# Optimization experiments

Hardware: AMD Instinct MI355X
Metric: run time of the kernel (lower is better)

The kernel has to match this reference:

```python
import jax, jax.numpy as jnp
import numpy as np

NUM_TRACKS = [5313, 1643, 128, 0]
MAX_TRACKS = max(NUM_TRACKS)
EMBED_DIM = 1536
LN_EPS = 1e-5


def setup_inputs() -> dict:
    key = jax.random.key(0)
    ks = jax.random.split(key, 8)
    B, S, D = 4, 896, EMBED_DIM
    inp = {
        "x": jax.random.normal(ks[0], (B, S, D), dtype=jnp.float32),
        "head_idx": jax.random.randint(ks[1], (B,), 0, 4, dtype=jnp.int64) if jax.config.jax_enable_x64 else jax.random.randint(ks[1], (B,), 0, 4).astype(jnp.int32),
    }
    for i, n in enumerate([5313, 1643, 128]):
        inp[f"gamma{i}"] = jnp.ones((D,), jnp.float32)
        inp[f"beta{i}"] = jnp.zeros((D,), jnp.float32)
        inp[f"W{i}"] = jax.random.normal(ks[2 + i], (n, D), dtype=jnp.float32) * 0.02
        inp[f"b{i}"] = jnp.zeros((n,), jnp.float32)
    return inp


def _linear_head(x, gamma, beta, W, b):
    # LayerNormFP32 -> Linear -> softplus, cast back to orig dtype
    orig_dtype = x.dtype
    xf = x.astype(jnp.float32)
    mu = jnp.mean(xf, axis=-1, keepdims=True)
    var = jnp.var(xf, axis=-1, keepdims=True)  # biased, as torch LayerNorm
    xn = (xf - mu) * jax.lax.rsqrt(var + LN_EPS) * gamma + beta
    h = jax.nn.softplus(jnp.einsum("bsd,td->bst", xn, W) + b)
    return h.astype(orig_dtype)


def reference(x, head_idx, gamma0, beta0, W0, b0,
              gamma1, beta1, W1, b1, gamma2, beta2, W2, b2):
    params = [(gamma0, beta0, W0, b0),
              (gamma1, beta1, W1, b1),
              (gamma2, beta2, W2, b2),
              None]  # ZeroHead
    B, S, _ = x.shape
    logits = jnp.zeros((B, S, MAX_TRACKS), dtype=x.dtype)
    for i, p in enumerate(params):
        if p is None:
            padded = jnp.zeros((B, S, MAX_TRACKS), dtype=x.dtype)
        else:
            h = _linear_head(x, *p)  # [B, S, n_i]
            pad = MAX_TRACKS - h.shape[-1]
            padded = jnp.pad(h, ((0, 0), (0, 0), (0, pad))) if pad > 0 else h
        mask = (head_idx == i)[:, None, None]
        logits = jnp.where(mask, padded, logits)
    return logits
```

## Files before the change

### kernel.cpp

```cpp
#include <hip/hip_runtime.h>
#include <hip/hip_bf16.h>

#define EMBED 1536
#define SEQ   896
#define NOUT  5313

#define N0 5313
#define N1 1643
#define N2 128
#define W0OFF 0
#define W1OFF 5376
#define W2OFF 7040
#define PTOT  7168

#define LN_BLOCKS 1792
#define WC_BLOCKS 5376
#define GEMM_GRID 1280
#define BK 128

typedef __attribute__((ext_vector_type(8))) short bf16x8;
typedef __attribute__((ext_vector_type(4))) float f32x4;

__device__ __forceinline__ void gload_lds16(const void* g, void* l) {
    __builtin_amdgcn_global_load_lds(
        (const __attribute__((address_space(1))) void*)g,
        (__attribute__((address_space(3))) void*)l, 16, 0, 0);
}

__device__ __forceinline__ int tiles_of(int h) {
    return (h == 0) ? 42 : (h == 1) ? 13 : (h == 2) ? 1 : 0;
}
__device__ __forceinline__ int nrows_of(int h) {
    return (h == 0) ? N0 : (h == 1) ? N1 : (h == 2) ? N2 : 0;
}

__global__ __launch_bounds__(256) void prep_kernel(
    const float* __restrict__ x, const int* __restrict__ head_idx,
    const float* __restrict__ g0, const float* __restrict__ be0,
    const float* __restrict__ g1, const float* __restrict__ be1,
    const float* __restrict__ g2, const float* __restrict__ be2,
    const float* __restrict__ W0, const float* __restrict__ W1,
    const float* __restrict__ W2,
    __hip_bfloat16* __restrict__ xn, __hip_bfloat16* __restrict__ wpad)
{
    const int tid = threadIdx.x;

    if (blockIdx.x < LN_BLOCKS) {
        const int half = tid >> 7;
        const int lt   = tid & 127;
        const int row  = blockIdx.x * 2 + half;
        const int b    = row / SEQ;
        const int h    = head_idx[b];
        if (h == 3) return;

        const float* gamma = (h == 1) ? g1 : (h == 2) ? g2 : g0;
        const float* beta  = (h == 1) ? be1 : (h == 2) ? be2 : be0;
        const float* xr = x + (size_t)row * EMBED;

        float4 v[3];
        float sum = 0.f, sq = 0.f;
#pragma unroll
        for (int i = 0; i < 3; ++i) {
            v[i] = ((const float4*)xr)[lt + i * 128];
            sum += v[i].x + v[i].y + v[i].z + v[i].w;
            sq  += v[i].x * v[i].x + v[i].y * v[i].y + v[i].z * v[i].z + v[i].w * v[i].w;
        }
#pragma unroll
        for (int off = 32; off > 0; off >>= 1) {
            sum += __shfl_down(sum, off);
            sq  += __shfl_down(sq, off);
        }
        __shared__ float s_sum[4], s_sq[4];
        const int wave = tid >> 6, lane = tid & 63;
        if (lane == 0) { s_sum[wave] = sum; s_sq[wave] = sq; }
        __syncthreads();
        const int wb = half << 1;
        const float mu  = (s_sum[wb] + s_sum[wb + 1]) * (1.f / EMBED);
        const float var = (s_sq[wb] + s_sq[wb + 1]) * (1.f / EMBED) - mu * mu;
        const float rs  = rsqrtf(var + 1e-5f);

        __hip_bfloat16* xo = xn + (size_t)row * EMBED;
#pragma unroll
        for (int i = 0; i < 3; ++i) {
            const int idx = lt + i * 128;
            float4 gv = ((const float4*)gamma)[idx];
            float4 bv = ((const float4*)beta)[idx];
            union { __hip_bfloat16 h4[4]; short4 s4; } u;
            u.h4[0] = __float2bfloat16((v[i].x - mu) * rs * gv.x + bv.x);
            u.h4[1] = __float2bfloat16((v[i].y - mu) * rs * gv.y + bv.y);
            u.h4[2] = __float2bfloat16((v[i].z - mu) * rs * gv.z + bv.z);
            u.h4[3] = __float2bfloat16((v[i].w - mu) * rs * gv.w + bv.w);
            ((short4*)xo)[idx] = u.s4;
        }
    } else {
        const int gid = (blockIdx.x - LN_BLOCKS) * 256 + tid;
        const int r = gid / 192;
        const int c = (gid - r * 192) * 8;
        const int region = (r < W1OFF) ? 0 : (r < W2OFF) ? 1 : 2;
        const int h0 = head_idx[0], h1 = head_idx[1];
        const int h2 = head_idx[2], h3 = head_idx[3];
        if (region != h0 && region != h1 && region != h2 && region != h3)
            return;
        const float* src = nullptr;
        if (region == 0)      { if (r < N0) src = W0 + (size_t)r * EMBED; }
        else if (region == 1) { int rr = r - W1OFF; if (rr < N1) src = W1 + (size_t)rr * EMBED; }
        else                  { int rr = r - W2OFF; if (rr < N2) src = W2 + (size_t)rr * EMBED; }
        union { __hip_bfloat16 h8[8]; int4 v4; } u;
        if (src) {
            float4 a = ((const float4*)(src + c))[0];
            float4 b = ((const float4*)(src + c))[1];
            u.h8[0] = __float2bfloat16(a.x); u.h8[1] = __float2bfloat16(a.y);
            u.h8[2] = __float2bfloat16(a.z); u.h8[3] = __float2bfloat16(a.w);
            u.h8[4] = __float2bfloat16(b.x); u.h8[5] = __float2bfloat16(b.y);
            u.h8[6] = __float2bfloat16(b.z); u.h8[7] = __float2bfloat16(b.w);
        } else {
            u.v4 = make_int4(0, 0, 0, 0);
        }
        *(int4*)(wpad + (size_t)r * EMBED + c) = u.v4;
    }
}

__global__ __launch_bounds__(256, 2) void head_gemm(
    const __hip_bfloat16* __restrict__ xn,
    const __hip_bfloat16* __restrict__ wpad,
    const float* __restrict__ b0, const float* __restrict__ b1,
    const float* __restrict__ b2,
    const int* __restrict__ head_idx,
    float* __restrict__ out)
{
    const int h0 = head_idx[0], h1 = head_idx[1];
    const int h2 = head_idx[2], h3 = head_idx[3];
    const int t0 = tiles_of(h0) * 7, t1 = tiles_of(h1) * 7;
    const int t2 = tiles_of(h2) * 7, t3 = tiles_of(h3) * 7;
    const int R = t0 + t1 + t2 + t3;
    const int tid = threadIdx.x;

    if ((int)blockIdx.x >= R) {
        const int j = blockIdx.x - R;
        const int ZB = GEMM_GRID - R;
        for (int row = j; row < 4 * SEQ; row += ZB) {
            const int b = row / SEQ;
            const int h = (b == 0) ? h0 : (b == 1) ? h1 : (b == 2) ? h2 : h3;
            const int n = nrows_of(h);
            if (n >= NOUT) continue;
            float* o = out + (size_t)row * NOUT;
            const int pre0 = (4 - (int)(((size_t)row * NOUT + n) & 3)) & 3;
            const int pre_end = min(n + pre0, NOUT);
            for (int c = n + tid; c < pre_end; c += 256) o[c] = 0.f;
            const int nvec = (NOUT - pre_end) >> 2;
            const float4 z = make_float4(0.f, 0.f, 0.f, 0.f);
            float4* ov = (float4*)(o + pre_end);
            for (int i = tid; i < nvec; i += 256) ov[i] = z;
            for (int c = pre_end + (nvec << 2) + tid; c < NOUT; c += 256) o[c] = 0.f;
        }
        return;
    }

    int rem = blockIdx.x, b;
    if (rem < t0)                { b = 0; }
    else if (rem < t0 + t1)      { b = 1; rem -= t0; }
    else if (rem < t0 + t1 + t2) { b = 2; rem -= t0 + t1; }
    else                         { b = 3; rem -= t0 + t1 + t2; }

    const int h = (b == 0) ? h0 : (b == 1) ? h1 : (b == 2) ? h2 : h3;
    const int ntc = tiles_of(h);
    const int mt = rem / ntc;
    const int nt = rem - mt * ntc;
    const int nrows = nrows_of(h);
    const int wbase = (h == 0) ? W0OFF : (h == 1) ? W1OFF : W2OFF;

    const int col0 = nt * 128;
    float* outb = out + ((size_t)b * SEQ + (size_t)mt * 128) * NOUT;

    __shared__ __hip_bfloat16 As[128 * BK];
    __shared__ __hip_bfloat16 Bs[128 * BK];
    const __hip_bfloat16* Ab = xn + ((size_t)b * SEQ + (size_t)mt * 128) * EMBED;
    const __hip_bfloat16* Bb = wpad + (size_t)(wbase + col0) * EMBED;

    const int wave = tid >> 6, lane = tid & 63;
    const int wm = wave >> 1, wn = wave & 1;
    const int fm = lane & 15, quad = lane >> 4;

    f32x4 acc[4][4] = {};

    for (int kt = 0; kt < EMBED / BK; ++kt) {
        const int k0 = kt * BK;
        __syncthreads();
#pragma unroll
        for (int i = 0; i < 8; ++i) {
            const int c = tid + i * 256;
            const int arow = c >> 4;
            const int kc = (c & 15) ^ (arow & 15);
            gload_lds16(Ab + (size_t)arow * EMBED + k0 + kc * 8, As + c * 8);
        }
#pragma unroll
        for (int i = 0; i < 8; ++i) {
            const int c = tid + i * 256;
            const int brow = c >> 4;
            const int kc = (c & 15) ^ (brow & 15);
            gload_lds16(Bb + (size_t)brow * EMBED + k0 + kc * 8, Bs + c * 8);
        }
        __syncthreads();
#pragma unroll
        for (int ks = 0; ks < 4; ++ks) {
            bf16x8 af[4], bfr[4];
#pragma unroll
            for (int i = 0; i < 4; ++i)
                af[i] = *(const bf16x8*)&As[(wm * 64 + i * 16 + fm) * BK +
                                            (((ks << 2) + quad) ^ fm) * 8];
#pragma unroll
            for (int j = 0; j < 4; ++j)
                bfr[j] = *(const bf16x8*)&Bs[(wn * 64 + j * 16 + fm) * BK +
                                             (((ks << 2) + quad) ^ fm) * 8];
#pragma unroll
            for (int i = 0; i < 4; ++i)
#pragma unroll
                for (int j = 0; j < 4; ++j)
                    acc[i][j] = __builtin_amdgcn_mfma_f32_16x16x32_bf16(
                        af[i], bfr[j], acc[i][j], 0, 0, 0);
        }
    }

    const float* bias = (h == 1) ? b1 : (h == 2) ? b2 : b0;
#pragma unroll
    for (int j = 0; j < 4; ++j) {
        const int lcol = col0 + wn * 64 + j * 16 + fm;
        const bool valid = lcol < nrows;
        const float bv = valid ? bias[lcol] : 0.f;
#pragma unroll
        for (int i = 0; i < 4; ++i) {
            const int rbase = wm * 64 + i * 16 + quad * 4;
#pragma unroll
            for (int r = 0; r < 4; ++r) {
                const float v = acc[i][j][r] + bv;
                const float sp = fmaxf(v, 0.f) + __logf(1.f + __expf(-fabsf(v)));
                if (valid) outb[(size_t)(rbase + r) * NOUT + lcol] = sp;
            }
        }
    }
}

extern "C" void kernel_launch(void* const* d_in, const int* in_sizes, int n_in,
                              void* d_out, int out_size, void* d_ws, size_t ws_size,
                              hipStream_t stream) {
    const float* x   = (const float*)d_in[0];
    const int* hidx  = (const int*)d_in[1];
    const float* g0  = (const float*)d_in[2];
    const float* be0 = (const float*)d_in[3];
    const float* W0  = (const float*)d_in[4];
    const float* b0  = (const float*)d_in[5];
    const float* g1  = (const float*)d_in[6];
    const float* be1 = (const float*)d_in[7];
    const float* W1  = (const float*)d_in[8];
    const float* b1  = (const float*)d_in[9];
    const float* g2  = (const float*)d_in[10];
    const float* be2 = (const float*)d_in[11];
    const float* W2  = (const float*)d_in[12];
    const float* b2  = (const float*)d_in[13];
    float* out = (float*)d_out;

    const size_t XN_BYTES = (size_t)4 * SEQ * EMBED * 2;
    __hip_bfloat16* xn   = (__hip_bfloat16*)d_ws;
    __hip_bfloat16* wpad = (__hip_bfloat16*)((char*)d_ws + XN_BYTES);

    prep_kernel<<<LN_BLOCKS + WC_BLOCKS, 256, 0, stream>>>(
        x, hidx, g0, be0, g1, be1, g2, be2, W0, W1, W2, xn, wpad);
    head_gemm<<<GEMM_GRID, 256, 0, stream>>>(xn, wpad, b0, b1, b2, hidx, out);
}
```

Before: 173.7 us.

## Double-buffer GEMM LDS tiles with BK=64 and remap blocks across XCDs

The GEMM main loop now uses two LDS buffers with a K-tile of 64, so the global-to-LDS loads for the next tile are issued before the MFMAs on the current tile, replacing the old load-sync-compute pattern. Block indices are also remapped so that consecutive tiles land on the same XCD, which is meant to improve L2 reuse of shared A and B rows. The price is more barriers per K (24 iterations instead of 12). LDS footprint stays the same, but relying on hand-written vmcnt waits and s_barrier adds a risk of ordering mistakes.

```diff
diff --git a/kernel.cpp b/kernel.cpp
--- a/kernel.cpp
+++ b/kernel.cpp
@@ -16,7 +16,8 @@
 #define LN_BLOCKS 1792
 #define WC_BLOCKS 5376
 #define GEMM_GRID 1280
-#define BK 128
+#define BK 64
+#define NKT (EMBED / BK)
 
 typedef __attribute__((ext_vector_type(8))) short bf16x8;
 typedef __attribute__((ext_vector_type(4))) float f32x4;
@@ -156,7 +157,11 @@
         return;
     }
 
-    int rem = blockIdx.x, b;
+    const int q = R >> 3, r7 = R & 7;
+    const int xcd = (int)blockIdx.x & 7, jx = (int)blockIdx.x >> 3;
+    const int tile = (xcd < r7 ? xcd * (q + 1) : r7 * (q + 1) + (xcd - r7) * q) + jx;
+
+    int rem = tile, b;
     if (rem < t0)                { b = 0; }
     else if (rem < t0 + t1)      { b = 1; rem -= t0; }
     else if (rem < t0 + t1 + t2) { b = 2; rem -= t0 + t1; }
@@ -172,8 +177,8 @@
     const int col0 = nt * 128;
     float* outb = out + ((size_t)b * SEQ + (size_t)mt * 128) * NOUT;
 
-    __shared__ __hip_bfloat16 As[128 * BK];
-    __shared__ __hip_bfloat16 Bs[128 * BK];
+    __shared__ __hip_bfloat16 As[2][128 * BK];
+    __shared__ __hip_bfloat16 Bs[2][128 * BK];
     const __hip_bfloat16* Ab = xn + ((size_t)b * SEQ + (size_t)mt * 128) * EMBED;
     const __hip_bfloat16* Bb = wpad + (size_t)(wbase + col0) * EMBED;
 
@@ -181,43 +186,54 @@
     const int wm = wave >> 1, wn = wave & 1;
     const int fm = lane & 15, quad = lane >> 4;
 
+    auto stage = [&](int buf, int kt) {
+        const int k0 = kt * BK;
+#pragma unroll
+        for (int i = 0; i < 4; ++i) {
+            const int c = tid + i * 256;
+            const int arow = c >> 3;
+            const int kc = (c & 7) ^ (arow & 7);
+            gload_lds16(Ab + (size_t)arow * EMBED + k0 + kc * 8, &As[buf][c * 8]);
+        }
+#pragma unroll
+        for (int i = 0; i < 4; ++i) {
+            const int c = tid + i * 256;
+            const int brow = c >> 3;
+            const int kc = (c & 7) ^ (brow & 7);
+            gload_lds16(Bb + (size_t)brow * EMBED + k0 + kc * 8, &Bs[buf][c * 8]);
+        }
+    };
+
     f32x4 acc[4][4] = {};
 
-    for (int kt = 0; kt < EMBED / BK; ++kt) {
-        const int k0 = kt * BK;
-        __syncthreads();
-#pragma unroll
-        for (int i = 0; i < 8; ++i) {
-            const int c = tid + i * 256;
-            const int arow = c >> 4;
-            const int kc = (c & 15) ^ (arow & 15);
-            gload_lds16(Ab + (size_t)arow * EMBED + k0 + kc * 8, As + c * 8);
-        }
-#pragma unroll
-        for (int i = 0; i < 8; ++i) {
-            const int c = tid + i * 256;
-            const int brow = c >> 4;
-            const int kc = (c & 15) ^ (brow & 15);
-            gload_lds16(Bb + (size_t)brow * EMBED + k0 + kc * 8, Bs + c * 8);
-        }
-        __syncthreads();
-#pragma unroll
-        for (int ks = 0; ks < 4; ++ks) {
+    stage(0, 0);
+    asm volatile("s_waitcnt vmcnt(0)" ::: "memory");
+    __builtin_amdgcn_s_barrier();
+
+    for (int kt = 0; kt < NKT; ++kt) {
+        const int cur = kt & 1;
+        if (kt + 1 < NKT) stage(cur ^ 1, kt + 1);
+#pragma unroll
+        for (int ks = 0; ks < 2; ++ks) {
             bf16x8 af[4], bfr[4];
 #pragma unroll
             for (int i = 0; i < 4; ++i)
-                af[i] = *(const bf16x8*)&As[(wm * 64 + i * 16 + fm) * BK +
-                                            (((ks << 2) + quad) ^ fm) * 8];
-#pragma unroll
-            for (int j = 0; j < 4; ++j)
-                bfr[j] = *(const bf16x8*)&Bs[(wn * 64 + j * 16 + fm) * BK +
-                                             (((ks << 2) + quad) ^ fm) * 8];
+                af[i] = *(const bf16x8*)&As[cur][(wm * 64 + i * 16 + fm) * BK +
+                                                ((((ks << 2) + quad)) ^ (fm & 7)) * 8];
+#pragma unroll
+            for (int j2 = 0; j2 < 4; ++j2)
+                bfr[j2] = *(const bf16x8*)&Bs[cur][(wn * 64 + j2 * 16 + fm) * BK +
+                                                  ((((ks << 2) + quad)) ^ (fm & 7)) * 8];
 #pragma unroll
             for (int i = 0; i < 4; ++i)
 #pragma unroll
-                for (int j = 0; j < 4; ++j)
-                    acc[i][j] = __builtin_amdgcn_mfma_f32_16x16x32_bf16(
-                        af[i], bfr[j], acc[i][j], 0, 0, 0);
+                for (int j2 = 0; j2 < 4; ++j2)
+                    acc[i][j2] = __builtin_amdgcn_mfma_f32_16x16x32_bf16(
+                        af[i], bfr[j2], acc[i][j2], 0, 0, 0);
+        }
+        if (kt + 1 < NKT) {
+            asm volatile("s_waitcnt vmcnt(0)" ::: "memory");
+            __builtin_amdgcn_s_barrier();
         }
     }
 
```

After: 175.9 us. About the same (+1.2%).
